# Performance work log

Hardware: AMD Instinct MI355X
Metric: run time of the kernel (lower is better)

The kernel has to match this reference:

```python
import jax, jax.numpy as jnp
from jax import lax
import numpy as np

IN_DIM, HID, B, T = 8, 50, 4096, 512

def setup_inputs() -> dict:
    key = jax.random.key(0)
    ks = jax.random.split(key, 8)
    s_ih = 1.0 / np.sqrt(HID)
    return {
        "x": jax.random.normal(ks[0], (B, T, IN_DIM), dtype=jnp.float32),
        "W_ih": jax.random.uniform(ks[1], (3 * HID, IN_DIM), jnp.float32, -s_ih, s_ih),
        "W_hh": jax.random.uniform(ks[2], (3 * HID, HID), jnp.float32, -s_ih, s_ih),
        "b_ih": jax.random.uniform(ks[3], (3 * HID,), jnp.float32, -s_ih, s_ih),
        "b_hh": jax.random.uniform(ks[4], (3 * HID,), jnp.float32, -s_ih, s_ih),
        "W_out": jax.random.uniform(ks[5], (1, HID), jnp.float32, -s_ih, s_ih),
        "b_out": jax.random.uniform(ks[6], (1,), jnp.float32, -s_ih, s_ih),
    }

def reference(x, W_ih, W_hh, b_ih, b_hh, W_out, b_out):
    # Precompute input projections for all timesteps: [B, T, 3H]
    xW = jnp.einsum('bti,gi->btg', x, W_ih) + b_ih

    def step(h, xw_t):  # h: [B, H], xw_t: [B, 3H]
        gi_r, gi_z, gi_n = jnp.split(xw_t, 3, axis=-1)
        gh = h @ W_hh.T + b_hh
        gh_r, gh_z, gh_n = jnp.split(gh, 3, axis=-1)
        r = jax.nn.sigmoid(gi_r + gh_r)
        z = jax.nn.sigmoid(gi_z + gh_z)
        n = jnp.tanh(gi_n + r * gh_n)
        h_new = (1.0 - z) * n + z * h
        return h_new, None

    h0 = jnp.zeros((x.shape[0], W_hh.shape[1]), dtype=x.dtype)
    hT, _ = lax.scan(step, h0, jnp.moveaxis(xW, 1, 0))  # scan over time
    # Linear head on final hidden state; torch squeezes the layer dim -> [B, 1]
    return hT @ W_out.T + b_out
```

## Files before the change

kernel.cpp:

```cpp
#include <hip/hip_runtime.h>

#define HID 50
#define IND 8
#define TLEN 512
#define NB 16
#define CH 128
#define XTS 136
#define NTHR 448

typedef _Float16 f16x8 __attribute__((ext_vector_type(8)));
typedef _Float16 f16x4 __attribute__((ext_vector_type(4)));
typedef _Float16 f16x2 __attribute__((ext_vector_type(2)));
typedef float f32x4 __attribute__((ext_vector_type(4)));

__global__ __launch_bounds__(NTHR, 1) void gru_mfma9(
    const float* __restrict__ x,
    const float* __restrict__ W_ih,
    const float* __restrict__ W_hh,
    const float* __restrict__ b_ih,
    const float* __restrict__ b_hh,
    const float* __restrict__ W_out,
    const float* __restrict__ b_out,
    float* __restrict__ out)
{
    const int tid  = threadIdx.x;
    const int wave = tid >> 6;
    const int lane = tid & 63;
    const int m16  = lane & 15;
    const int quad = lane >> 4;
    const int bb   = blockIdx.x;

    const int t0  = 2 * wave;
    const int t1  = 2 * wave + 1;
    const int jh0 = 8 * wave + quad;
    const int jh1 = 8 * wave + 4 + quad;

    __shared__ _Float16 B_lds[2 * 896];
    __shared__ _Float16 x_frag[CH * XTS];
    __shared__ float    red[NB * 56];

    const int P[8] = {0, 4, 1, 5, 2, 6, 3, 7};

    auto aval = [&](int tt, int k) -> float {
        const int R  = 16 * tt + m16;
        const int rj = R >> 2;
        const int g  = R & 3;
        if (rj >= HID) return 0.f;
        const float sc = (g <= 1) ? -1.44269504f : 2.88539008f;
        float w = 0.f;
        if (g <= 1) {
            if (k < HID)      w = W_hh[(g * HID + rj) * HID + k];
            else if (k >= 56) w = W_ih[(g * HID + rj) * IND + (k - 56)];
        } else if (g == 2) {
            if (k < HID)      w = W_hh[(2 * HID + rj) * HID + k];
        } else {
            if (k >= 56)      w = W_ih[(2 * HID + rj) * IND + (k - 56)];
        }
        return sc * w;
    };

    f16x8 a00, a01, a10, a11;
#pragma unroll
    for (int p = 0; p < 8; ++p) {
        a00[p] = (_Float16)aval(t0, quad * 8 + P[p]);
        a01[p] = (_Float16)aval(t0, 32 + quad * 8 + P[p]);
        a10[p] = (_Float16)aval(t1, quad * 8 + P[p]);
        a11[p] = (_Float16)aval(t1, 32 + quad * 8 + P[p]);
    }

    auto mkbias = [&](int jh) -> f32x4 {
        f32x4 b = {0.f, 0.f, 0.f, 0.f};
        if (jh < HID) {
            b[0] = -1.44269504f * (b_ih[jh] + b_hh[jh]);
            b[1] = -1.44269504f * (b_ih[HID + jh] + b_hh[HID + jh]);
            b[2] =  2.88539008f * b_hh[2 * HID + jh];
            b[3] =  2.88539008f * b_ih[2 * HID + jh];
        }
        return b;
    };
    const f32x4 bias0 = mkbias(jh0);
    const f32x4 bias1 = mkbias(jh1);

    float h0 = 0.f, h1 = 0.f;

    auto stage_chunk = [&](int c) {
        for (int u = tid; u < NB * CH; u += NTHR) {
            const int n    = u >> 7;
            const int trel = u & (CH - 1);
            const float4* s = (const float4*)(x + ((size_t)(bb * NB + n) * TLEN + (size_t)c * CH + trel) * IND);
            const float4 va = s[0];
            const float4 vb = s[1];
            const f16x4 lo = {(_Float16)va.x, (_Float16)vb.x, (_Float16)va.y, (_Float16)vb.y};
            const f16x4 hi = {(_Float16)va.z, (_Float16)vb.z, (_Float16)va.w, (_Float16)vb.w};
            *(f16x4*)&x_frag[trel * XTS + n * 8]     = lo;
            *(f16x4*)&x_frag[trel * XTS + n * 8 + 4] = hi;
        }
    };

    for (int idx = tid; idx < 2 * 896; idx += NTHR)
        B_lds[idx] = (_Float16)0.f;
    stage_chunk(0);
    __syncthreads();

    const int lane8 = lane * 8;
    const _Float16* xq = &x_frag[m16 * 8];
    const int wad = wave * 128 + m16 * 8 + 2 * quad;

    auto gates = [&](const f32x4& cc, float h) -> float {
        const float R2 = __builtin_amdgcn_exp2f(cc[0]);
        const float r  = __builtin_amdgcn_rcpf(1.0f + R2);
        const float Z2 = __builtin_amdgcn_exp2f(cc[1]);
        const float E  = __builtin_amdgcn_exp2f(cc[3] + r * cc[2]);
        const float num = E * (Z2 + h) + (h - Z2);
        const float den = (E + 1.0f) * (Z2 + 1.0f);
        return num * __builtin_amdgcn_rcpf(den);
    };

    auto step = [&](int i, int cur, int nxt) {
        _Float16* Bc = &B_lds[cur * 896];
        _Float16* Bn = &B_lds[nxt * 896];
        const f16x8 bf0 = *(const f16x8*)(Bc + lane8);
        const _Float16* p1 = (quad == 3) ? (xq + (size_t)i * XTS) : (Bc + 512 + lane8);
        const f16x8 bf1 = *(const f16x8*)p1;
        f32x4 c0 = __builtin_amdgcn_mfma_f32_16x16x32_f16(a00, bf0, bias0, 0, 0, 0);
        f32x4 c1 = __builtin_amdgcn_mfma_f32_16x16x32_f16(a10, bf0, bias1, 0, 0, 0);
        c0 = __builtin_amdgcn_mfma_f32_16x16x32_f16(a01, bf1, c0, 0, 0, 0);
        c1 = __builtin_amdgcn_mfma_f32_16x16x32_f16(a11, bf1, c1, 0, 0, 0);
        h0 = gates(c0, h0);
        h1 = gates(c1, h1);
        *(f16x2*)(Bn + wad) = f16x2{(_Float16)h0, (_Float16)h1};
        __syncthreads();
    };

    for (int c = 0; c < 4; ++c) {
        if (c != 0) { stage_chunk(c); __syncthreads(); }
#pragma unroll 4
        for (int i = 0; i < CH; i += 2) {
            step(i,     0, 1);
            step(i + 1, 1, 0);
        }
    }

    if (jh0 < HID) red[m16 * 56 + jh0] = h0 * W_out[jh0];
    if (jh1 < HID) red[m16 * 56 + jh1] = h1 * W_out[jh1];
    __syncthreads();
    if (tid < NB) {
        float s = b_out[0];
        for (int j = 0; j < HID; ++j) s += red[tid * 56 + j];
        out[bb * NB + tid] = s;
    }
}

extern "C" void kernel_launch(void* const* d_in, const int* in_sizes, int n_in,
                              void* d_out, int out_size, void* d_ws, size_t ws_size,
                              hipStream_t stream) {
    const float* x     = (const float*)d_in[0];
    const float* W_ih  = (const float*)d_in[1];
    const float* W_hh  = (const float*)d_in[2];
    const float* b_ih  = (const float*)d_in[3];
    const float* b_hh  = (const float*)d_in[4];
    const float* W_out = (const float*)d_in[5];
    const float* b_out = (const float*)d_in[6];
    float* out = (float*)d_out;

    const int B = in_sizes[0] / (TLEN * IND);
    gru_mfma9<<<B / NB, NTHR, 0, stream>>>(x, W_ih, W_hh, b_ih, b_hh, W_out, b_out, out);
}
```

Measured before the change: 232.8 us.

## Replace per-step block barrier with LDS flag point-to-point wave synchronization

Each timestep no longer ends in a workgroup-wide __syncthreads. Instead every wave publishes a per-wave step counter in LDS after its hidden-state write drains. Before each read, consumer waves spin until the specific producer waves they depend on have reached the current step. The goal is to let waves proceed as soon as their inputs are ready, removing full-barrier latency from the serial recurrence. The cost is spin-polling overhead and a possible write-after-read hazard on the double-buffered state. The unroll factor also drops from 4 to 2.

New measurement: 265.5 us. 1.14x slower.

```diff
diff --git a/kernel.cpp b/kernel.cpp
--- a/kernel.cpp
+++ b/kernel.cpp
@@ -13,7 +13,7 @@
 typedef _Float16 f16x2 __attribute__((ext_vector_type(2)));
 typedef float f32x4 __attribute__((ext_vector_type(4)));
 
-__global__ __launch_bounds__(NTHR, 1) void gru_mfma9(
+__global__ __launch_bounds__(NTHR, 1) void gru_mfma14(
     const float* __restrict__ x,
     const float* __restrict__ W_ih,
     const float* __restrict__ W_hh,
@@ -38,6 +38,7 @@
     __shared__ _Float16 B_lds[2 * 896];
     __shared__ _Float16 x_frag[CH * XTS];
     __shared__ float    red[NB * 56];
+    __shared__ int      wflag[7 * 8];
 
     const int P[8] = {0, 4, 1, 5, 2, 6, 3, 7};
 
@@ -99,6 +100,7 @@
 
     for (int idx = tid; idx < 2 * 896; idx += NTHR)
         B_lds[idx] = (_Float16)0.f;
+    if (tid < 56) wflag[tid] = 0;
     stage_chunk(0);
     __syncthreads();
 
@@ -106,20 +108,28 @@
     const _Float16* xq = &x_frag[m16 * 8];
     const int wad = wave * 128 + m16 * 8 + 2 * quad;
 
-    auto gates = [&](const f32x4& cc, float h) -> float {
+    const int l3 = lane & 3;
+    volatile int* pfA = (volatile int*)&wflag[l3 * 8];
+    volatile int* pfB = (volatile int*)&wflag[(4 + (l3 == 3 ? 0 : l3)) * 8];
+
+    auto gates = [&](const f32x4& cc, float hh) -> float {
         const float R2 = __builtin_amdgcn_exp2f(cc[0]);
         const float r  = __builtin_amdgcn_rcpf(1.0f + R2);
         const float Z2 = __builtin_amdgcn_exp2f(cc[1]);
         const float E  = __builtin_amdgcn_exp2f(cc[3] + r * cc[2]);
-        const float num = E * (Z2 + h) + (h - Z2);
+        const float num = E * (Z2 + hh) + (hh - Z2);
         const float den = (E + 1.0f) * (Z2 + 1.0f);
         return num * __builtin_amdgcn_rcpf(den);
     };
 
-    auto step = [&](int i, int cur, int nxt) {
+    auto step = [&](int i, int cur, int nxt, int tgt) {
         _Float16* Bc = &B_lds[cur * 896];
         _Float16* Bn = &B_lds[nxt * 896];
+        while (__any(*pfA < tgt)) {}
+        asm volatile("" ::: "memory");
         const f16x8 bf0 = *(const f16x8*)(Bc + lane8);
+        while (__any(*pfB < tgt)) {}
+        asm volatile("" ::: "memory");
         const _Float16* p1 = (quad == 3) ? (xq + (size_t)i * XTS) : (Bc + 512 + lane8);
         const f16x8 bf1 = *(const f16x8*)p1;
         f32x4 c0 = __builtin_amdgcn_mfma_f32_16x16x32_f16(a00, bf0, bias0, 0, 0, 0);
@@ -129,15 +139,22 @@
         h0 = gates(c0, h0);
         h1 = gates(c1, h1);
         *(f16x2*)(Bn + wad) = f16x2{(_Float16)h0, (_Float16)h1};
-        __syncthreads();
+        asm volatile("s_waitcnt lgkmcnt(0)" ::: "memory");
+        if (lane == 0) *(volatile int*)&wflag[wave * 8] = tgt + 1;
     };
 
+    int gt = 0;
     for (int c = 0; c < 4; ++c) {
-        if (c != 0) { stage_chunk(c); __syncthreads(); }
-#pragma unroll 4
+        if (c != 0) {
+            __syncthreads();
+            stage_chunk(c);
+            __syncthreads();
+        }
+#pragma unroll 2
         for (int i = 0; i < CH; i += 2) {
-            step(i,     0, 1);
-            step(i + 1, 1, 0);
+            step(i,     0, 1, gt);
+            step(i + 1, 1, 0, gt + 1);
+            gt += 2;
         }
     }
 
@@ -164,5 +181,5 @@
     float* out = (float*)d_out;
 
     const int B = in_sizes[0] / (TLEN * IND);
-    gru_mfma9<<<B / NB, NTHR, 0, stream>>>(x, W_ih, W_hh, b_ih, b_hh, W_out, b_out, out);
+    gru_mfma14<<<B / NB, NTHR, 0, stream>>>(x, W_ih, W_hh, b_ih, b_hh, W_out, b_out, out);
 }
```
